# Optimization experiments

Measured on AMD Instinct MI355X. Metric: run time of the kernel, lower is better.

Reference implementation:

```python
import jax, jax.numpy as jnp
import numpy as np

B, T, D_IN = 2, 2048, 1024
H, D_HEAD = 16, 64
D_INNER = H * D_HEAD  # 1024
D_OUT = D_HEAD        # out_proj maps d_inner -> d_out


def setup_inputs() -> dict:
    key = jax.random.key(0)
    ks = jax.random.split(key, 6)
    s_in = 1.0 / np.sqrt(D_IN)
    s_inner = 1.0 / np.sqrt(D_INNER)
    return {
        "x": jax.random.normal(ks[0], (B, T, D_IN), dtype=jnp.float32),
        "Wq": jax.random.uniform(ks[1], (D_IN, D_INNER), jnp.float32, -s_in, s_in),
        "Wk": jax.random.uniform(ks[2], (D_IN, D_INNER), jnp.float32, -s_in, s_in),
        "Wv": jax.random.uniform(ks[3], (D_IN, D_INNER), jnp.float32, -s_in, s_in),
        "Wo": jax.random.uniform(ks[4], (D_INNER, D_OUT), jnp.float32, -s_inner, s_inner),
        "bo": jax.random.uniform(ks[5], (D_OUT,), jnp.float32, -s_inner, s_inner),
    }


def reference(x, Wq, Wk, Wv, Wo, bo):
    b, t, _ = x.shape
    # projections -> [b, h, t, d]
    def split_heads(y):
        return y.reshape(b, t, H, D_HEAD).transpose(0, 2, 1, 3)
    q = split_heads(x @ Wq)
    k = split_heads(x @ Wk)
    v = split_heads(x @ Wv)
    scores = jnp.einsum("bhqd,bhkd->bhqk", q, k)
    causal = jnp.triu(jnp.ones((t, t), dtype=bool), k=1)
    scores = jnp.where(causal, -jnp.inf, scores)
    # NOTE: original scales by sqrt(d_out*num_heads), not sqrt(head_dim)
    attn = jax.nn.softmax(scores / np.sqrt(D_INNER), axis=-1)
    y = jnp.einsum("bhqk,bhkd->bhqd", attn, v)
    y = y.transpose(0, 2, 1, 3).reshape(b, t, D_INNER)
    return y @ Wo + bo
```

## Files before the change

kernel.cpp:

```cpp
#include <hip/hip_runtime.h>

typedef __attribute__((ext_vector_type(8))) short short8;
typedef __attribute__((ext_vector_type(4))) float f32x4;
typedef __attribute__((ext_vector_type(8))) unsigned short ushort8v;


__device__ __forceinline__ unsigned short f2bf(float f) {
  union { float f; unsigned int u; } x; x.f = f;
  unsigned int r = x.u + 0x7FFFu + ((x.u >> 16) & 1u);
  return (unsigned short)(r >> 16);
}

__device__ __forceinline__ void gload_lds16(const void* g, void* l) {
  __builtin_amdgcn_global_load_lds(
      (const __attribute__((address_space(1))) void*)g,
      (__attribute__((address_space(3))) void*)l, 16, 0, 0);
}


__global__ __launch_bounds__(256) void prep(
    const float* __restrict__ x,
    const float* __restrict__ Wq, const float* __restrict__ Wk, const float* __restrict__ Wv,
    const float* __restrict__ Wo, const float* __restrict__ bo,
    unsigned short* __restrict__ xb,
    unsigned short* __restrict__ wqt, unsigned short* __restrict__ wkt,
    unsigned short* __restrict__ wvt, unsigned short* __restrict__ wot,
    float* __restrict__ out) {
  __shared__ float tile[32][33];
  int b = blockIdx.x;
  if (b < 4096) {
    int i = (b * 256 + threadIdx.x) * 4;
    float4 f = *(const float4*)(x + i);
    ushort4 o;
    o.x = f2bf(f.x); o.y = f2bf(f.y); o.z = f2bf(f.z); o.w = f2bf(f.w);
    *(ushort4*)(xb + i) = o;
  } else if (b < 7168) {
    int idx = b - 4096;
    int z = idx >> 10, rem = idx & 1023;
    const float* src = (z == 0) ? Wq : (z == 1) ? Wk : Wv;
    unsigned short* dst = (z == 0) ? wqt : (z == 1) ? wkt : wvt;
    int kx = (rem & 31) * 32, ny = (rem >> 5) * 32;
    int tx = threadIdx.x & 31, ty = threadIdx.x >> 5;
    #pragma unroll
    for (int r = 0; r < 32; r += 8)
      tile[ty + r][tx] = src[(size_t)(kx + ty + r) * 1024 + ny + tx];
    __syncthreads();
    #pragma unroll
    for (int r = 0; r < 32; r += 8)
      dst[(size_t)(ny + ty + r) * 1024 + kx + tx] = f2bf(tile[tx][ty + r]);
  } else if (b < 7232) {
    int idx = b - 7168;
    int kx = (idx & 31) * 32, ny = (idx >> 5) * 32;
    int tx = threadIdx.x & 31, ty = threadIdx.x >> 5;
    #pragma unroll
    for (int r = 0; r < 32; r += 8)
      tile[ty + r][tx] = Wo[(size_t)(kx + ty + r) * 64 + ny + tx];
    __syncthreads();
    #pragma unroll
    for (int r = 0; r < 32; r += 8)
      wot[(size_t)(ny + ty + r) * 1024 + kx + tx] = f2bf(tile[tx][ty + r]);
  } else {
    int t = (b - 7232) * 256 + threadIdx.x;
    float4 bi = *(const float4*)(bo + (t & 15) * 4);
    *(float4*)(out + (size_t)t * 4) = bi;
  }
}


__global__ __launch_bounds__(256) void qkv_gemm(
    const unsigned short* __restrict__ Xb,
    const unsigned short* __restrict__ Wqt, const unsigned short* __restrict__ Wkt,
    const unsigned short* __restrict__ Wvt,
    unsigned short* __restrict__ Oq, unsigned short* __restrict__ Ok,
    unsigned short* __restrict__ Ovt) {
  constexpr int Kd = 1024;
  __shared__ __align__(16) unsigned short As[128 * 64];
  __shared__ __align__(16) unsigned short Bs[128 * 64];
  int z = blockIdx.z;
  int m0, n0;
  const unsigned short *Arow, *Brow;
  if (z == 2) {
    m0 = blockIdx.x * 128; n0 = blockIdx.y * 128;
    Arow = Xb; Brow = Wvt;
  } else {
    m0 = blockIdx.y * 128; n0 = blockIdx.x * 128;
    Arow = (z == 0) ? Wqt : Wkt; Brow = Xb;
  }
  int tid = threadIdx.x, lane = tid & 63, wave = tid >> 6;
  int wm = wave >> 1, wn = wave & 1;
  int l15 = lane & 15, quad = lane >> 4;
  int swz = l15 & 7;

  f32x4 acc[4][4] = {};

  for (int k0 = 0; k0 < Kd; k0 += 64) {
    __syncthreads();
    #pragma unroll
    for (int r = 0; r < 4; ++r) {
      int i = tid + 256 * r;
      int row = i >> 3, c8 = i & 7;
      int gc8 = c8 ^ (row & 7);
      gload_lds16(Arow + (size_t)(m0 + row) * Kd + k0 + gc8 * 8, &As[i * 8]);
    }
    #pragma unroll
    for (int r = 0; r < 4; ++r) {
      int i = tid + 256 * r;
      int row = i >> 3, c8 = i & 7;
      int gc8 = c8 ^ (row & 7);
      gload_lds16(Brow + (size_t)(n0 + row) * Kd + k0 + gc8 * 8, &Bs[i * 8]);
    }
    __syncthreads();
    short8 af[4][2], bf[4][2];
    #pragma unroll
    for (int s = 0; s < 2; ++s) {
      #pragma unroll
      for (int i = 0; i < 4; ++i)
        af[i][s] = *(const short8*)&As[(wm * 64 + i * 16 + l15) * 64 + (((s << 2) + quad) ^ swz) * 8];
      #pragma unroll
      for (int j = 0; j < 4; ++j)
        bf[j][s] = *(const short8*)&Bs[(wn * 64 + j * 16 + l15) * 64 + (((s << 2) + quad) ^ swz) * 8];
    }
    #pragma unroll
    for (int s = 0; s < 2; ++s)
      #pragma unroll
      for (int i = 0; i < 4; ++i)
        #pragma unroll
        for (int j = 0; j < 4; ++j)
          acc[i][j] = __builtin_amdgcn_mfma_f32_16x16x32_bf16(af[i][s], bf[j][s], acc[i][j], 0, 0, 0);
  }

  if (z == 2) {
    #pragma unroll
    for (int i = 0; i < 4; ++i) {
      int tbase = m0 + wm * 64 + i * 16 + quad * 4;
      int b = tbase >> 11, tt = tbase & 2047;
      #pragma unroll
      for (int j = 0; j < 4; ++j) {
        int dm = n0 + wn * 64 + j * 16 + l15;
        int h = dm >> 6, d = dm & 63;
        unsigned int u0 = f2bf(acc[i][j][0]), u1 = f2bf(acc[i][j][1]);
        unsigned int u2 = f2bf(acc[i][j][2]), u3 = f2bf(acc[i][j][3]);
        uint2 pk; pk.x = u0 | (u1 << 16); pk.y = u2 | (u3 << 16);
        *(uint2*)(Ovt + (((size_t)(b * 16 + h) * 64 + d) << 11) + tt) = pk;
      }
    }
  } else {
    unsigned short* O = (z == 0) ? Oq : Ok;
    float scale = (z == 0) ? 0.0450842200f : 1.0f;
    #pragma unroll
    for (int i = 0; i < 4; ++i) {
      int dmbase = m0 + wm * 64 + i * 16 + quad * 4;
      int h = dmbase >> 6, d0 = dmbase & 63;
      #pragma unroll
      for (int j = 0; j < 4; ++j) {
        int t = n0 + wn * 64 + j * 16 + l15;
        int b = t >> 11, tt = t & 2047;
        unsigned int u0 = f2bf(acc[i][j][0] * scale), u1 = f2bf(acc[i][j][1] * scale);
        unsigned int u2 = f2bf(acc[i][j][2] * scale), u3 = f2bf(acc[i][j][3] * scale);
        uint2 pk; pk.x = u0 | (u1 << 16); pk.y = u2 | (u3 << 16);
        *(uint2*)(O + (((size_t)(b * 16 + h) * 2048 + tt) << 6) + d0) = pk;
      }
    }
  }
}


__global__ __launch_bounds__(256, 4) void attn11(
    const unsigned short* __restrict__ Qg, const unsigned short* __restrict__ Kg,
    const unsigned short* __restrict__ Vtg, unsigned short* __restrict__ Yg) {
  constexpr int T = 2048;
  __shared__ __align__(16) unsigned short Ks[2][64 * 64];
  __shared__ __align__(16) unsigned short Vs[2][64 * 64];
  __shared__ __align__(16) unsigned short Ps[4][16 * 64];
  int bh = blockIdx.x;
  int by = blockIdx.y;
  int g = by >> 3, w8 = by & 7;
  int qt = (g == 0) ? w8 : (g == 1) ? (15 - w8) : (g == 2) ? (16 + w8) : (31 - w8);
  int tid = threadIdx.x, lane = tid & 63, wave = tid >> 6;
  int l15 = lane & 15, quad = lane >> 4;
  int swz = l15 & 7;
  const unsigned short* Qb = Qg + (size_t)bh * T * 64;
  const unsigned short* Kb = Kg + (size_t)bh * T * 64;
  const unsigned short* Vb = Vtg + (size_t)bh * 64 * T;
  int h = bh & 15, b = bh >> 4;
  int qw = qt * 64 + wave * 16;

  short8 qf[2];
  #pragma unroll
  for (int s = 0; s < 2; ++s)
    qf[s] = *(const short8*)(Qb + (size_t)(qw + l15) * 64 + quad * 8 + 32 * s);

  f32x4 Oacc[4] = {};
  float m_run = -__builtin_inff();
  float l_run = 0.f;

  int srow = tid >> 3, sc8 = tid & 7;
  int sdst = srow * 64 + ((sc8 ^ (srow & 7)) * 8);

  ushort8v kpre[2], vpre[2];
  #pragma unroll
  for (int r = 0; r < 2; ++r) {
    kpre[r] = *(const ushort8v*)(Kb + (size_t)(srow + 32 * r) * 64 + sc8 * 8);
    vpre[r] = *(const ushort8v*)(Vb + (size_t)(srow + 32 * r) * T + sc8 * 8);
  }
  *(ushort8v*)&Ks[0][sdst] = kpre[0];
  *(ushort8v*)&Ks[0][sdst + 2048] = kpre[1];
  *(ushort8v*)&Vs[0][sdst] = vpre[0];
  *(ushort8v*)&Vs[0][sdst + 2048] = vpre[1];
  __syncthreads();

  for (int kt = 0; kt <= qt; ++kt) {
    const unsigned short* Kl = Ks[kt & 1];
    const unsigned short* Vl = Vs[kt & 1];
    unsigned short* Kn = Ks[(kt & 1) ^ 1];
    unsigned short* Vn = Vs[(kt & 1) ^ 1];

    if (kt < qt) {
      #pragma unroll
      for (int r = 0; r < 2; ++r) {
        kpre[r] = *(const ushort8v*)(Kb + (size_t)((kt + 1) * 64 + srow + 32 * r) * 64 + sc8 * 8);
        vpre[r] = *(const ushort8v*)(Vb + (size_t)(srow + 32 * r) * T + (kt + 1) * 64 + sc8 * 8);
      }
    }

    f32x4 S[4] = {};
    __builtin_amdgcn_s_setprio(1);
    #pragma unroll
    for (int s = 0; s < 2; ++s)
      #pragma unroll
      for (int mi = 0; mi < 4; ++mi) {
        short8 kf = *(const short8*)&Kl[(mi * 16 + l15) * 64 + ((quad + 4 * s) ^ swz) * 8];
        S[mi] = __builtin_amdgcn_mfma_f32_16x16x32_bf16(kf, qf[s], S[mi], 0, 0, 0);
      }
    __builtin_amdgcn_s_setprio(0);

    if (kt == qt) {
      int ql = wave * 16 + l15;
      #pragma unroll
      for (int mi = 0; mi < 4; ++mi) {
        int tokl = mi * 16 + quad * 4;
        #pragma unroll
        for (int r = 0; r < 4; ++r)
          if (tokl + r > ql) S[mi][r] = -__builtin_inff();
      }
    }

    float t0 = fmaxf(fmaxf(S[0][0], S[0][1]), fmaxf(S[0][2], S[0][3]));
    float t1 = fmaxf(fmaxf(S[1][0], S[1][1]), fmaxf(S[1][2], S[1][3]));
    float t2 = fmaxf(fmaxf(S[2][0], S[2][1]), fmaxf(S[2][2], S[2][3]));
    float t3 = fmaxf(fmaxf(S[3][0], S[3][1]), fmaxf(S[3][2], S[3][3]));
    float vmax = fmaxf(fmaxf(t0, t1), fmaxf(t2, t3));
    vmax = fmaxf(vmax, __shfl_xor(vmax, 16));
    vmax = fmaxf(vmax, __shfl_xor(vmax, 32));
    float mold = m_run;
    bool defer = __all(vmax - mold <= 8.f) != 0;
    float mnew = defer ? mold : fmaxf(mold, vmax);
    float alpha = defer ? 1.f : __builtin_amdgcn_exp2f(mold - mnew);
    m_run = mnew;
    float rs = 0.f;
    #pragma unroll
    for (int mi = 0; mi < 4; ++mi) {
      float p0 = __builtin_amdgcn_exp2f(S[mi][0] - mnew);
      float p1 = __builtin_amdgcn_exp2f(S[mi][1] - mnew);
      float p2 = __builtin_amdgcn_exp2f(S[mi][2] - mnew);
      float p3 = __builtin_amdgcn_exp2f(S[mi][3] - mnew);
      rs += (p0 + p1) + (p2 + p3);
      union { float f; unsigned int u; } a0{p0}, a1{p1}, a2{p2}, a3{p3};
      uint2 pk;
      pk.x = ((a0.u + 0x8000u) >> 16) | ((a1.u + 0x8000u) & 0xFFFF0000u);
      pk.y = ((a2.u + 0x8000u) >> 16) | ((a3.u + 0x8000u) & 0xFFFF0000u);
      int gg = (2 * mi + (quad >> 1)) ^ swz;
      *(uint2*)&Ps[wave][l15 * 64 + gg * 8 + (quad & 1) * 4] = pk;
    }
    rs += __shfl_xor(rs, 16);
    rs += __shfl_xor(rs, 32);
    l_run = l_run * alpha + rs;

    if (!defer)
      #pragma unroll
      for (int jd = 0; jd < 4; ++jd)
        #pragma unroll
        for (int r = 0; r < 4; ++r)
          Oacc[jd][r] *= alpha;

    if (kt < qt) {
      *(ushort8v*)&Kn[sdst] = kpre[0];
      *(ushort8v*)&Kn[sdst + 2048] = kpre[1];
      *(ushort8v*)&Vn[sdst] = vpre[0];
      *(ushort8v*)&Vn[sdst + 2048] = vpre[1];
    }

    __builtin_amdgcn_s_setprio(1);
    #pragma unroll
    for (int s = 0; s < 2; ++s) {
      short8 pf = *(const short8*)&Ps[wave][l15 * 64 + ((quad + 4 * s) ^ swz) * 8];
      #pragma unroll
      for (int jd = 0; jd < 4; ++jd) {
        short8 vfr = *(const short8*)&Vl[(jd * 16 + l15) * 64 + ((quad + 4 * s) ^ swz) * 8];
        Oacc[jd] = __builtin_amdgcn_mfma_f32_16x16x32_bf16(vfr, pf, Oacc[jd], 0, 0, 0);
      }
    }
    __builtin_amdgcn_s_setprio(0);
    if (kt < qt) __syncthreads();
  }

  {
    float linv = 1.f / l_run;
    int q = qw + l15;
    size_t row = (size_t)(b * 2048 + q) * 1024 + h * 64 + quad * 4;
    #pragma unroll
    for (int jd = 0; jd < 4; ++jd) {
      unsigned int u0 = f2bf(Oacc[jd][0] * linv), u1 = f2bf(Oacc[jd][1] * linv);
      unsigned int u2 = f2bf(Oacc[jd][2] * linv), u3 = f2bf(Oacc[jd][3] * linv);
      uint2 pk; pk.x = u0 | (u1 << 16); pk.y = u2 | (u3 << 16);
      *(uint2*)(Yg + row + jd * 16) = pk;
    }
  }
}


__global__ __launch_bounds__(256) void oproj(
    const unsigned short* __restrict__ Y, const unsigned short* __restrict__ Wot,
    float* __restrict__ out) {
  __shared__ __align__(16) unsigned short As[64 * 32];
  __shared__ __align__(16) unsigned short Bs[64 * 32];
  int m0 = blockIdx.x * 64;
  int kbase = blockIdx.y * 256;
  int tid = threadIdx.x, lane = tid & 63, wave = tid >> 6;
  int l15 = lane & 15, quad = lane >> 4;
  f32x4 acc[4] = {};
  for (int k0 = kbase; k0 < kbase + 256; k0 += 32) {
    __syncthreads();
    {
      int row = tid >> 2, c8 = (tid & 3) * 8;
      gload_lds16(Y + (size_t)(m0 + row) * 1024 + k0 + c8, &As[tid * 8]);
      gload_lds16(Wot + (size_t)row * 1024 + k0 + c8, &Bs[tid * 8]);
    }
    __syncthreads();
    short8 af = *(const short8*)&As[(wave * 16 + l15) * 32 + quad * 8];
    #pragma unroll
    for (int j = 0; j < 4; ++j) {
      short8 bf = *(const short8*)&Bs[(j * 16 + l15) * 32 + quad * 8];
      acc[j] = __builtin_amdgcn_mfma_f32_16x16x32_bf16(af, bf, acc[j], 0, 0, 0);
    }
  }
  #pragma unroll
  for (int j = 0; j < 4; ++j) {
    int n = j * 16 + l15;
    #pragma unroll
    for (int r = 0; r < 4; ++r) {
      int m = m0 + wave * 16 + quad * 4 + r;
      atomicAdd(&out[(size_t)m * 64 + n], acc[j][r]);
    }
  }
}


extern "C" void kernel_launch(void* const* d_in, const int* in_sizes, int n_in,
                              void* d_out, int out_size, void* d_ws, size_t ws_size,
                              hipStream_t stream) {
  const float* x  = (const float*)d_in[0];
  const float* Wq = (const float*)d_in[1];
  const float* Wk = (const float*)d_in[2];
  const float* Wv = (const float*)d_in[3];
  const float* Wo = (const float*)d_in[4];
  const float* bo = (const float*)d_in[5];
  float* out = (float*)d_out;
  char* ws = (char*)d_ws;

  unsigned short* xb  = (unsigned short*)(ws);
  unsigned short* wqt = (unsigned short*)(ws + (8ull << 20));
  unsigned short* wkt = (unsigned short*)(ws + (10ull << 20));
  unsigned short* wvt = (unsigned short*)(ws + (12ull << 20));
  unsigned short* wot = (unsigned short*)(ws + (14ull << 20));
  unsigned short* q   = (unsigned short*)(ws + (15ull << 20));
  unsigned short* k   = (unsigned short*)(ws + (23ull << 20));
  unsigned short* vt  = (unsigned short*)(ws + (31ull << 20));
  unsigned short* y   = (unsigned short*)(ws + (39ull << 20));

  prep<<<7488, 256, 0, stream>>>(x, Wq, Wk, Wv, Wo, bo, xb, wqt, wkt, wvt, wot, out);
  qkv_gemm<<<dim3(32, 8, 3), 256, 0, stream>>>(xb, wqt, wkt, wvt, q, k, vt);
  attn11<<<dim3(32, 32), 256, 0, stream>>>(q, k, vt, y);
  oproj<<<dim3(64, 4), 256, 0, stream>>>(y, wot, out);
}
```

Before: 159.0 us.

## Software-pipeline QK^T one tile ahead of softmax and PV in attention

The attention loop now computes the next tile's QK^T scores while the current tile's softmax and PV run, and it prefetches K/V two tiles ahead. The prologue loads the first two tiles and computes the first scores. The aim is to overlap MFMA work with the exp/max VALU work and to hide global load latency. This costs extra registers for the Sn scores, which can hurt occupancy at 4 blocks per CU, and adds a second barrier per iteration. The hand-written bf16 packing is replaced with the HIP __float22bfloat162_rn intrinsic, which also changes rounding from round-half-up to round-to-nearest-even.

```diff
diff --git a/kernel.cpp b/kernel.cpp
--- a/kernel.cpp
+++ b/kernel.cpp
@@ -1,4 +1,5 @@
 #include <hip/hip_runtime.h>
+#include <hip/hip_bf16.h>
 
 typedef __attribute__((ext_vector_type(8))) short short8;
 typedef __attribute__((ext_vector_type(4))) float f32x4;
@@ -9,6 +10,12 @@
   union { float f; unsigned int u; } x; x.f = f;
   unsigned int r = x.u + 0x7FFFu + ((x.u >> 16) & 1u);
   return (unsigned short)(r >> 16);
+}
+
+__device__ __forceinline__ unsigned int pk2bf(float lo, float hi) {
+  __hip_bfloat162 b2 = __float22bfloat162_rn(make_float2(lo, hi));
+  union { __hip_bfloat162 b; unsigned int u; } c; c.b = b2;
+  return c.u;
 }
 
 __device__ __forceinline__ void gload_lds16(const void* g, void* l) {
@@ -165,7 +172,7 @@
 }
 
 
-__global__ __launch_bounds__(256, 4) void attn11(
+__global__ __launch_bounds__(256, 4) void attn12(
     const unsigned short* __restrict__ Qg, const unsigned short* __restrict__ Kg,
     const unsigned short* __restrict__ Vtg, unsigned short* __restrict__ Yg) {
   constexpr int T = 2048;
@@ -197,42 +204,59 @@
   int srow = tid >> 3, sc8 = tid & 7;
   int sdst = srow * 64 + ((sc8 ^ (srow & 7)) * 8);
 
+  {
+    ushort8v kA[2], vA[2], kB[2], vB[2];
+    #pragma unroll
+    for (int r = 0; r < 2; ++r) {
+      kA[r] = *(const ushort8v*)(Kb + (size_t)(srow + 32 * r) * 64 + sc8 * 8);
+      vA[r] = *(const ushort8v*)(Vb + (size_t)(srow + 32 * r) * T + sc8 * 8);
+      kB[r] = *(const ushort8v*)(Kb + (size_t)(64 + srow + 32 * r) * 64 + sc8 * 8);
+      vB[r] = *(const ushort8v*)(Vb + (size_t)(srow + 32 * r) * T + 64 + sc8 * 8);
+    }
+    *(ushort8v*)&Ks[0][sdst] = kA[0];
+    *(ushort8v*)&Ks[0][sdst + 2048] = kA[1];
+    *(ushort8v*)&Vs[0][sdst] = vA[0];
+    *(ushort8v*)&Vs[0][sdst + 2048] = vA[1];
+    *(ushort8v*)&Ks[1][sdst] = kB[0];
+    *(ushort8v*)&Ks[1][sdst + 2048] = kB[1];
+    *(ushort8v*)&Vs[1][sdst] = vB[0];
+    *(ushort8v*)&Vs[1][sdst + 2048] = vB[1];
+  }
+  __syncthreads();
+
+  f32x4 S[4] = {};
+  #pragma unroll
+  for (int s = 0; s < 2; ++s)
+    #pragma unroll
+    for (int mi = 0; mi < 4; ++mi) {
+      short8 kf = *(const short8*)&Ks[0][(mi * 16 + l15) * 64 + ((quad + 4 * s) ^ swz) * 8];
+      S[mi] = __builtin_amdgcn_mfma_f32_16x16x32_bf16(kf, qf[s], S[mi], 0, 0, 0);
+    }
+
   ushort8v kpre[2], vpre[2];
-  #pragma unroll
-  for (int r = 0; r < 2; ++r) {
-    kpre[r] = *(const ushort8v*)(Kb + (size_t)(srow + 32 * r) * 64 + sc8 * 8);
-    vpre[r] = *(const ushort8v*)(Vb + (size_t)(srow + 32 * r) * T + sc8 * 8);
-  }
-  *(ushort8v*)&Ks[0][sdst] = kpre[0];
-  *(ushort8v*)&Ks[0][sdst + 2048] = kpre[1];
-  *(ushort8v*)&Vs[0][sdst] = vpre[0];
-  *(ushort8v*)&Vs[0][sdst + 2048] = vpre[1];
-  __syncthreads();
-
   for (int kt = 0; kt <= qt; ++kt) {
-    const unsigned short* Kl = Ks[kt & 1];
-    const unsigned short* Vl = Vs[kt & 1];
-    unsigned short* Kn = Ks[(kt & 1) ^ 1];
-    unsigned short* Vn = Vs[(kt & 1) ^ 1];
-
-    if (kt < qt) {
+    int cur = kt & 1;
+    bool haveNext = (kt + 1 <= qt);
+    bool haveNext2 = (kt + 2 <= qt);
+
+    if (haveNext2) {
       #pragma unroll
       for (int r = 0; r < 2; ++r) {
-        kpre[r] = *(const ushort8v*)(Kb + (size_t)((kt + 1) * 64 + srow + 32 * r) * 64 + sc8 * 8);
-        vpre[r] = *(const ushort8v*)(Vb + (size_t)(srow + 32 * r) * T + (kt + 1) * 64 + sc8 * 8);
+        kpre[r] = *(const ushort8v*)(Kb + (size_t)((kt + 2) * 64 + srow + 32 * r) * 64 + sc8 * 8);
+        vpre[r] = *(const ushort8v*)(Vb + (size_t)(srow + 32 * r) * T + (kt + 2) * 64 + sc8 * 8);
       }
     }
 
-    f32x4 S[4] = {};
-    __builtin_amdgcn_s_setprio(1);
-    #pragma unroll
-    for (int s = 0; s < 2; ++s)
-      #pragma unroll
-      for (int mi = 0; mi < 4; ++mi) {
-        short8 kf = *(const short8*)&Kl[(mi * 16 + l15) * 64 + ((quad + 4 * s) ^ swz) * 8];
-        S[mi] = __builtin_amdgcn_mfma_f32_16x16x32_bf16(kf, qf[s], S[mi], 0, 0, 0);
-      }
-    __builtin_amdgcn_s_setprio(0);
+    f32x4 Sn[4] = {};
+    if (haveNext) {
+      #pragma unroll
+      for (int s = 0; s < 2; ++s)
+        #pragma unroll
+        for (int mi = 0; mi < 4; ++mi) {
+          short8 kf = *(const short8*)&Ks[cur ^ 1][(mi * 16 + l15) * 64 + ((quad + 4 * s) ^ swz) * 8];
+          Sn[mi] = __builtin_amdgcn_mfma_f32_16x16x32_bf16(kf, qf[s], Sn[mi], 0, 0, 0);
+        }
+    }
 
     if (kt == qt) {
       int ql = wave * 16 + l15;
@@ -265,10 +289,9 @@
       float p2 = __builtin_amdgcn_exp2f(S[mi][2] - mnew);
       float p3 = __builtin_amdgcn_exp2f(S[mi][3] - mnew);
       rs += (p0 + p1) + (p2 + p3);
-      union { float f; unsigned int u; } a0{p0}, a1{p1}, a2{p2}, a3{p3};
       uint2 pk;
-      pk.x = ((a0.u + 0x8000u) >> 16) | ((a1.u + 0x8000u) & 0xFFFF0000u);
-      pk.y = ((a2.u + 0x8000u) >> 16) | ((a3.u + 0x8000u) & 0xFFFF0000u);
+      pk.x = pk2bf(p0, p1);
+      pk.y = pk2bf(p2, p3);
       int gg = (2 * mi + (quad >> 1)) ^ swz;
       *(uint2*)&Ps[wave][l15 * 64 + gg * 8 + (quad & 1) * 4] = pk;
     }
@@ -283,25 +306,31 @@
         for (int r = 0; r < 4; ++r)
           Oacc[jd][r] *= alpha;
 
-    if (kt < qt) {
-      *(ushort8v*)&Kn[sdst] = kpre[0];
-      *(ushort8v*)&Kn[sdst + 2048] = kpre[1];
-      *(ushort8v*)&Vn[sdst] = vpre[0];
-      *(ushort8v*)&Vn[sdst + 2048] = vpre[1];
-    }
-
     __builtin_amdgcn_s_setprio(1);
     #pragma unroll
     for (int s = 0; s < 2; ++s) {
       short8 pf = *(const short8*)&Ps[wave][l15 * 64 + ((quad + 4 * s) ^ swz) * 8];
       #pragma unroll
       for (int jd = 0; jd < 4; ++jd) {
-        short8 vfr = *(const short8*)&Vl[(jd * 16 + l15) * 64 + ((quad + 4 * s) ^ swz) * 8];
+        short8 vfr = *(const short8*)&Vs[cur][(jd * 16 + l15) * 64 + ((quad + 4 * s) ^ swz) * 8];
         Oacc[jd] = __builtin_amdgcn_mfma_f32_16x16x32_bf16(vfr, pf, Oacc[jd], 0, 0, 0);
       }
     }
     __builtin_amdgcn_s_setprio(0);
-    if (kt < qt) __syncthreads();
+
+    if (haveNext2) {
+      __syncthreads();
+      *(ushort8v*)&Ks[cur][sdst] = kpre[0];
+      *(ushort8v*)&Ks[cur][sdst + 2048] = kpre[1];
+      *(ushort8v*)&Vs[cur][sdst] = vpre[0];
+      *(ushort8v*)&Vs[cur][sdst + 2048] = vpre[1];
+      __syncthreads();
+    }
+
+    if (haveNext) {
+      #pragma unroll
+      for (int mi = 0; mi < 4; ++mi) S[mi] = Sn[mi];
+    }
   }
 
   {
@@ -380,6 +409,6 @@
 
   prep<<<7488, 256, 0, stream>>>(x, Wq, Wk, Wv, Wo, bo, xb, wqt, wkt, wvt, wot, out);
   qkv_gemm<<<dim3(32, 8, 3), 256, 0, stream>>>(xb, wqt, wkt, wvt, q, k, vt);
-  attn11<<<dim3(32, 32), 256, 0, stream>>>(q, k, vt, y);
+  attn12<<<dim3(32, 32), 256, 0, stream>>>(q, k, vt, y);
   oproj<<<dim3(64, 4), 256, 0, stream>>>(y, wot, out);
 }
```

Result: slower. 164.5 us (+3.5%).

## Fuse output projection into attention epilogue with per-head atomic accumulation

Applied to the files above, without the earlier changes.

Removes the separate oproj kernel. Each attention wave normalizes its output tile, writes it as bf16 into its own LDS P-buffer, multiplies it by that head's slice of Wo with MFMA, and atomically adds into the fp32 output. This avoids the Y round-trip through global memory and one kernel launch. In exchange the number of atomics grows, with 16 heads contributing to each output element instead of 4 K-splits. The P-to-bf16 packing also switches to the hardware round-to-nearest conversion intrinsic.

```diff
diff --git a/kernel.cpp b/kernel.cpp
--- a/kernel.cpp
+++ b/kernel.cpp
@@ -1,4 +1,5 @@
 #include <hip/hip_runtime.h>
+#include <hip/hip_bf16.h>
 
 typedef __attribute__((ext_vector_type(8))) short short8;
 typedef __attribute__((ext_vector_type(4))) float f32x4;
@@ -9,6 +10,12 @@
   union { float f; unsigned int u; } x; x.f = f;
   unsigned int r = x.u + 0x7FFFu + ((x.u >> 16) & 1u);
   return (unsigned short)(r >> 16);
+}
+
+__device__ __forceinline__ unsigned int pk2bf(float lo, float hi) {
+  __hip_bfloat162 b2 = __float22bfloat162_rn(make_float2(lo, hi));
+  union { __hip_bfloat162 b; unsigned int u; } c; c.b = b2;
+  return c.u;
 }
 
 __device__ __forceinline__ void gload_lds16(const void* g, void* l) {
@@ -165,9 +172,10 @@
 }
 
 
-__global__ __launch_bounds__(256, 4) void attn11(
+__global__ __launch_bounds__(256, 4) void attn13(
     const unsigned short* __restrict__ Qg, const unsigned short* __restrict__ Kg,
-    const unsigned short* __restrict__ Vtg, unsigned short* __restrict__ Yg) {
+    const unsigned short* __restrict__ Vtg, const unsigned short* __restrict__ Wot,
+    float* __restrict__ out) {
   constexpr int T = 2048;
   __shared__ __align__(16) unsigned short Ks[2][64 * 64];
   __shared__ __align__(16) unsigned short Vs[2][64 * 64];
@@ -265,10 +273,9 @@
       float p2 = __builtin_amdgcn_exp2f(S[mi][2] - mnew);
       float p3 = __builtin_amdgcn_exp2f(S[mi][3] - mnew);
       rs += (p0 + p1) + (p2 + p3);
-      union { float f; unsigned int u; } a0{p0}, a1{p1}, a2{p2}, a3{p3};
       uint2 pk;
-      pk.x = ((a0.u + 0x8000u) >> 16) | ((a1.u + 0x8000u) & 0xFFFF0000u);
-      pk.y = ((a2.u + 0x8000u) >> 16) | ((a3.u + 0x8000u) & 0xFFFF0000u);
+      pk.x = pk2bf(p0, p1);
+      pk.y = pk2bf(p2, p3);
       int gg = (2 * mi + (quad >> 1)) ^ swz;
       *(uint2*)&Ps[wave][l15 * 64 + gg * 8 + (quad & 1) * 4] = pk;
     }
@@ -306,52 +313,35 @@
 
   {
     float linv = 1.f / l_run;
-    int q = qw + l15;
-    size_t row = (size_t)(b * 2048 + q) * 1024 + h * 64 + quad * 4;
+    unsigned short* Yl = &Ps[wave][0];
     #pragma unroll
     for (int jd = 0; jd < 4; ++jd) {
-      unsigned int u0 = f2bf(Oacc[jd][0] * linv), u1 = f2bf(Oacc[jd][1] * linv);
-      unsigned int u2 = f2bf(Oacc[jd][2] * linv), u3 = f2bf(Oacc[jd][3] * linv);
-      uint2 pk; pk.x = u0 | (u1 << 16); pk.y = u2 | (u3 << 16);
-      *(uint2*)(Yg + row + jd * 16) = pk;
-    }
-  }
-}
-
-
-__global__ __launch_bounds__(256) void oproj(
-    const unsigned short* __restrict__ Y, const unsigned short* __restrict__ Wot,
-    float* __restrict__ out) {
-  __shared__ __align__(16) unsigned short As[64 * 32];
-  __shared__ __align__(16) unsigned short Bs[64 * 32];
-  int m0 = blockIdx.x * 64;
-  int kbase = blockIdx.y * 256;
-  int tid = threadIdx.x, lane = tid & 63, wave = tid >> 6;
-  int l15 = lane & 15, quad = lane >> 4;
-  f32x4 acc[4] = {};
-  for (int k0 = kbase; k0 < kbase + 256; k0 += 32) {
-    __syncthreads();
-    {
-      int row = tid >> 2, c8 = (tid & 3) * 8;
-      gload_lds16(Y + (size_t)(m0 + row) * 1024 + k0 + c8, &As[tid * 8]);
-      gload_lds16(Wot + (size_t)row * 1024 + k0 + c8, &Bs[tid * 8]);
-    }
-    __syncthreads();
-    short8 af = *(const short8*)&As[(wave * 16 + l15) * 32 + quad * 8];
-    #pragma unroll
-    for (int j = 0; j < 4; ++j) {
-      short8 bf = *(const short8*)&Bs[(j * 16 + l15) * 32 + quad * 8];
-      acc[j] = __builtin_amdgcn_mfma_f32_16x16x32_bf16(af, bf, acc[j], 0, 0, 0);
-    }
-  }
-  #pragma unroll
-  for (int j = 0; j < 4; ++j) {
-    int n = j * 16 + l15;
-    #pragma unroll
-    for (int r = 0; r < 4; ++r) {
-      int m = m0 + wave * 16 + quad * 4 + r;
-      atomicAdd(&out[(size_t)m * 64 + n], acc[j][r]);
-    }
+      uint2 pk;
+      pk.x = pk2bf(Oacc[jd][0] * linv, Oacc[jd][1] * linv);
+      pk.y = pk2bf(Oacc[jd][2] * linv, Oacc[jd][3] * linv);
+      int gg = (jd * 2 + (quad >> 1)) ^ swz;
+      *(uint2*)&Yl[l15 * 64 + gg * 8 + (quad & 1) * 4] = pk;
+    }
+    short8 wof[4][2];
+    #pragma unroll
+    for (int nt = 0; nt < 4; ++nt)
+      #pragma unroll
+      for (int s = 0; s < 2; ++s)
+        wof[nt][s] = *(const short8*)(Wot + (size_t)(nt * 16 + l15) * 1024 + h * 64 + quad * 8 + 32 * s);
+    f32x4 acc2[4] = {};
+    #pragma unroll
+    for (int s = 0; s < 2; ++s) {
+      short8 ya = *(const short8*)&Yl[l15 * 64 + (((quad + 4 * s) ^ swz) * 8)];
+      #pragma unroll
+      for (int nt = 0; nt < 4; ++nt)
+        acc2[nt] = __builtin_amdgcn_mfma_f32_16x16x32_bf16(ya, wof[nt][s], acc2[nt], 0, 0, 0);
+    }
+    int q0 = b * 2048 + qt * 64 + wave * 16 + quad * 4;
+    #pragma unroll
+    for (int nt = 0; nt < 4; ++nt)
+      #pragma unroll
+      for (int r = 0; r < 4; ++r)
+        atomicAdd(&out[(size_t)(q0 + r) * 64 + nt * 16 + l15], acc2[nt][r]);
   }
 }
 
@@ -376,10 +366,8 @@
   unsigned short* q   = (unsigned short*)(ws + (15ull << 20));
   unsigned short* k   = (unsigned short*)(ws + (23ull << 20));
   unsigned short* vt  = (unsigned short*)(ws + (31ull << 20));
-  unsigned short* y   = (unsigned short*)(ws + (39ull << 20));
 
   prep<<<7488, 256, 0, stream>>>(x, Wq, Wk, Wv, Wo, bo, xb, wqt, wkt, wvt, wot, out);
   qkv_gemm<<<dim3(32, 8, 3), 256, 0, stream>>>(xb, wqt, wkt, wvt, q, k, vt);
-  attn11<<<dim3(32, 32), 256, 0, stream>>>(q, k, vt, y);
-  oproj<<<dim3(64, 4), 256, 0, stream>>>(y, wot, out);
-}
+  attn13<<<dim3(32, 32), 256, 0, stream>>>(q, k, vt, wot, out);
+}
```

After: 153.7 us. 1.03x faster.
